# Optimization experiments

Measured on AMD Instinct MI355X. Metric: run time of the kernel, lower is better.

## Reference

```python
import jax, jax.numpy as jnp
import numpy as np

N = 50000      # nodes per graph
E = 800000     # edges per graph
IN_DIM = 64
HIDDEN = 128
OUT_DIM = 2
P = 100000     # candidate residue pairs


def setup_inputs() -> dict:
    key = jax.random.key(0)
    ks = jax.random.split(key, 12)
    x1 = jax.random.normal(ks[0], (N, IN_DIM), dtype=jnp.float32)
    x2 = jax.random.normal(ks[1], (N, IN_DIM), dtype=jnp.float32)
    edge_index1 = jax.random.randint(ks[2], (2, E), 0, N, dtype=jnp.int64)
    edge_index2 = jax.random.randint(ks[3], (2, E), 0, N, dtype=jnp.int64)
    label = jax.random.randint(ks[4], (P, 2), 0, N, dtype=jnp.int64)
    s = 0.05
    W0 = jax.random.normal(ks[5], (IN_DIM, HIDDEN), dtype=jnp.float32) * s
    W1 = jax.random.normal(ks[6], (HIDDEN, HIDDEN), dtype=jnp.float32) * s
    W2 = jax.random.normal(ks[7], (HIDDEN, HIDDEN), dtype=jnp.float32) * s
    b0 = jnp.zeros((HIDDEN,), dtype=jnp.float32)
    b1 = jnp.zeros((HIDDEN,), dtype=jnp.float32)
    b2 = jnp.zeros((HIDDEN,), dtype=jnp.float32)
    fcW = jax.random.normal(ks[8], (2 * HIDDEN, OUT_DIM), dtype=jnp.float32) * s
    fcb = jnp.zeros((OUT_DIM,), dtype=jnp.float32)
    return {"x1": x1, "edge_index1": edge_index1, "x2": x2,
            "edge_index2": edge_index2, "label": label,
            "W0": W0, "b0": b0, "W1": W1, "b1": b1, "W2": W2, "b2": b2,
            "fcW": fcW, "fcb": fcb}


def gcn_conv(x, src, dst, W, b):
    """PyG GCNConv: linear, add self-loops, symmetric D^-1/2 (A+I) D^-1/2 aggregation."""
    n = x.shape[0]
    h = x @ W                                   # [n, out]
    loops = jnp.arange(n, dtype=src.dtype)
    src_sl = jnp.concatenate([src, loops])      # [E+n]
    dst_sl = jnp.concatenate([dst, loops])
    deg = jax.ops.segment_sum(jnp.ones_like(src_sl, dtype=h.dtype), dst_sl,
                              num_segments=n)
    dinv = jax.lax.rsqrt(jnp.maximum(deg, 1.0e-12))
    norm = dinv[src_sl] * dinv[dst_sl]          # [E+n]
    msgs = h[src_sl] * norm[:, None]            # gather + scale
    out = jax.ops.segment_sum(msgs, dst_sl, num_segments=n)  # scatter-add
    return out + b


def gcn_tower(x, edge_index, params):
    src, dst = edge_index[0], edge_index[1]
    for (W, b) in params:
        x = jax.nn.relu(gcn_conv(x, src, dst, W, b))
    return x


def reference(x1, edge_index1, x2, edge_index2, label,
              W0, b0, W1, b1, W2, b2, fcW, fcb):
    params = [(W0, b0), (W1, b1), (W2, b2)]
    x_ligand = gcn_tower(x1, edge_index1, params)    # shared GCN weights
    x_receptor = gcn_tower(x2, edge_index2, params)
    x = jnp.concatenate([x_ligand[label[:, 0]], x_receptor[label[:, 1]]], axis=1)
    return jax.nn.relu(x @ fcW + fcb)
```

## Files before the change

kernel.cpp:

```cpp
#include <hip/hip_runtime.h>
#include <math.h>

typedef __attribute__((ext_vector_type(8))) short bf16x8;
typedef __attribute__((ext_vector_type(4))) float f32x4;

__device__ inline unsigned short f2bf(float f) {
    unsigned int u = __float_as_uint(f);
    unsigned int r = u + 0x7fffu + ((u >> 16) & 1u);
    return (unsigned short)(r >> 16);
}
__device__ inline float bf2f(unsigned short b) {
    return __uint_as_float(((unsigned int)b) << 16);
}


__global__ void histU_kernel(const int* __restrict__ d1, const int* __restrict__ d2,
                             int* __restrict__ cnt, int E, int N) {
    int i = blockIdx.x * blockDim.x + threadIdx.x;
    if (i < E) atomicAdd(&cnt[d1[i]], 1);
    else if (i < 2 * E) atomicAdd(&cnt[N + d2[i - E]], 1);
}

__global__ __launch_bounds__(256) void block_reduce_kernel(const int* __restrict__ cnt,
                                                           float* __restrict__ dinv,
                                                           int* __restrict__ blockSums, int NN) {
    int i = blockIdx.x * 256 + threadIdx.x;
    int v = 0;
    if (i < NN) {
        v = cnt[i];
        dinv[i] = 1.0f / sqrtf((float)(v + 1));
    }
    int s = v;
#pragma unroll
    for (int o = 32; o; o >>= 1) s += __shfl_down(s, o);
    __shared__ int ws[4];
    if ((threadIdx.x & 63) == 0) ws[threadIdx.x >> 6] = s;
    __syncthreads();
    if (threadIdx.x == 0) blockSums[blockIdx.x] = ws[0] + ws[1] + ws[2] + ws[3];
}

__global__ __launch_bounds__(1024) void scan_sums_kernel(const int* __restrict__ blockSums,
                                                         int* __restrict__ blockOff, int nb,
                                                         int* __restrict__ rowptr, int NN) {
    __shared__ int sh[1024];
    int t = threadIdx.x;
    int v = (t < nb) ? blockSums[t] : 0;
    sh[t] = v;
    __syncthreads();
    for (int o = 1; o < 1024; o <<= 1) {
        int u = (t >= o) ? sh[t - o] : 0;
        __syncthreads();
        sh[t] += u;
        __syncthreads();
    }
    if (t < nb) blockOff[t] = sh[t] - v;
    if (t == 1023) rowptr[NN] = sh[1023];
}

__global__ __launch_bounds__(256) void scan_write_kernel(const int* __restrict__ cnt,
                                                         const int* __restrict__ blockOff,
                                                         int* __restrict__ rowptr, int NN) {
    __shared__ int sh[256];
    int i = blockIdx.x * 256 + threadIdx.x;
    int t = threadIdx.x;
    int v = (i < NN) ? cnt[i] : 0;
    sh[t] = v;
    __syncthreads();
    for (int o = 1; o < 256; o <<= 1) {
        int u = (t >= o) ? sh[t - o] : 0;
        __syncthreads();
        sh[t] += u;
        __syncthreads();
    }
    if (i < NN) rowptr[i] = blockOff[blockIdx.x] + sh[t] - v;
}

__global__ void placeU_kernel(const int* __restrict__ s1, const int* __restrict__ d1,
                              const int* __restrict__ s2, const int* __restrict__ d2,
                              const int* __restrict__ rowptr, int* __restrict__ cnt,
                              int* __restrict__ csr, int E, int N) {
    int i = blockIdx.x * blockDim.x + threadIdx.x;
    int s, d;
    if (i < E)          { s = s1[i];         d = d1[i]; }
    else if (i < 2 * E) { s = s2[i - E] + N; d = d2[i - E] + N; }
    else return;
    int p = atomicSub(&cnt[d], 1);
    csr[rowptr[d] + p - 1] = s;
}


__global__ void prep_weights(const float* __restrict__ W0, const float* __restrict__ W1,
                             const float* __restrict__ W2,
                             unsigned short* __restrict__ W0h, unsigned short* __restrict__ W0l,
                             unsigned short* __restrict__ W1h, unsigned short* __restrict__ W1l,
                             unsigned short* __restrict__ W2h, unsigned short* __restrict__ W2l) {
    const float* W; unsigned short *Wh, *Wl; int K;
    if (blockIdx.x == 0)      { W = W0; Wh = W0h; Wl = W0l; K = 64; }
    else if (blockIdx.x == 1) { W = W1; Wh = W1h; Wl = W1l; K = 128; }
    else                      { W = W2; Wh = W2h; Wl = W2l; K = 128; }
    for (int i = threadIdx.x; i < K * 128; i += 256) {
        int k = i >> 7, c = i & 127;
        float v = W[i];
        unsigned short h = f2bf(v);
        unsigned short l = f2bf(v - bf2f(h));
        Wh[c * K + k] = h;
        Wl[c * K + k] = l;
    }
}


__global__ void prescale_kernel(const float* __restrict__ x1, const float* __restrict__ x2,
                                const float* __restrict__ dinv, float* __restrict__ X0, int NN,
                                int N) {
    int i = blockIdx.x * blockDim.x + threadIdx.x;
    if (i >= NN * 16) return;
    int r = i >> 4;
    const float4* src = (r < N) ? (const float4*)(x1) + i
                                : (const float4*)(x2) + (i - N * 16);
    float4 v = *src;
    float d = dinv[r];
    v.x *= d; v.y *= d; v.z *= d; v.w *= d;
    reinterpret_cast<float4*>(X0)[i] = v;
}


__global__ __launch_bounds__(512) void fused64_agg_gemm(
    const float* __restrict__ X, const int* __restrict__ rowptr,
    const int* __restrict__ csr,
    const unsigned short* __restrict__ WhT, const unsigned short* __restrict__ WlT,
    const float* __restrict__ bias, const float* __restrict__ dinv, int post,
    float* __restrict__ C, int M) {
    const int K = 64;
    const int LDA = K + 8;
    __shared__ unsigned short ldsH[64 * LDA];
    __shared__ unsigned short ldsL[64 * LDA];

    int t = threadIdx.x;
    int lane = t & 63, wid = t >> 6;
    int row0 = blockIdx.x * 64;

    const float4* X4 = (const float4*)X;
    int grp = lane >> 4;
    int fl = lane & 15;

    for (int rr = 0; rr < 2; ++rr) {
        int row = wid * 8 + rr * 4 + grp;
        int g = row0 + row; if (g >= M) g = M - 1;
        int beg = rowptr[g], end = rowptr[g + 1];
        float4 s4 = X4[(size_t)g * 16 + fl];
        float a0 = s4.x, a1 = s4.y, a2 = s4.z, a3 = s4.w;
        int e = beg;
        while (end - e >= 8) {
            int s0 = csr[e], s1 = csr[e + 1], s2 = csr[e + 2], s3 = csr[e + 3];
            int s4i = csr[e + 4], s5 = csr[e + 5], s6 = csr[e + 6], s7 = csr[e + 7];
            float4 v0 = X4[(size_t)s0 * 16 + fl];
            float4 v1 = X4[(size_t)s1 * 16 + fl];
            float4 v2 = X4[(size_t)s2 * 16 + fl];
            float4 v3 = X4[(size_t)s3 * 16 + fl];
            float4 v4 = X4[(size_t)s4i * 16 + fl];
            float4 v5 = X4[(size_t)s5 * 16 + fl];
            float4 v6 = X4[(size_t)s6 * 16 + fl];
            float4 v7 = X4[(size_t)s7 * 16 + fl];
            a0 += ((v0.x + v1.x) + (v2.x + v3.x)) + ((v4.x + v5.x) + (v6.x + v7.x));
            a1 += ((v0.y + v1.y) + (v2.y + v3.y)) + ((v4.y + v5.y) + (v6.y + v7.y));
            a2 += ((v0.z + v1.z) + (v2.z + v3.z)) + ((v4.z + v5.z) + (v6.z + v7.z));
            a3 += ((v0.w + v1.w) + (v2.w + v3.w)) + ((v4.w + v5.w) + (v6.w + v7.w));
            e += 8;
        }
        if (e < end) {
#pragma unroll
            for (int j = 0; j < 7; ++j) {
                int a = e + j;
                bool vld = a < end;
                int s = csr[vld ? a : beg];
                float m = vld ? 1.f : 0.f;
                float4 v = X4[(size_t)s * 16 + fl];
                a0 += m * v.x; a1 += m * v.y; a2 += m * v.z; a3 += m * v.w;
            }
        }
        ushort4 H, L;
        H.x = f2bf(a0); L.x = f2bf(a0 - bf2f(H.x));
        H.y = f2bf(a1); L.y = f2bf(a1 - bf2f(H.y));
        H.z = f2bf(a2); L.z = f2bf(a2 - bf2f(H.z));
        H.w = f2bf(a3); L.w = f2bf(a3 - bf2f(H.w));
        *reinterpret_cast<ushort4*>(&ldsH[row * LDA + fl * 4]) = H;
        *reinterpret_cast<ushort4*>(&ldsL[row * LDA + fl * 4]) = L;
    }
    __syncthreads();

    int c16 = lane & 15, kq = (lane >> 4) * 8;
    int col = wid * 16 + c16;

    bf16x8 wh[K / 32], wl[K / 32];
#pragma unroll
    for (int ks = 0; ks < K / 32; ++ks) {
        wh[ks] = *reinterpret_cast<const bf16x8*>(WhT + (size_t)col * K + ks * 32 + kq);
        wl[ks] = *reinterpret_cast<const bf16x8*>(WlT + (size_t)col * K + ks * 32 + kq);
    }
    float bb = bias[col];

#pragma unroll
    for (int rt = 0; rt < 4; ++rt) {
        f32x4 acc = {0.f, 0.f, 0.f, 0.f};
        int abase = (rt * 16 + c16) * LDA + kq;
#pragma unroll
        for (int ks = 0; ks < K / 32; ++ks) {
            bf16x8 ah = *reinterpret_cast<const bf16x8*>(ldsH + abase + ks * 32);
            bf16x8 al = *reinterpret_cast<const bf16x8*>(ldsL + abase + ks * 32);
            acc = __builtin_amdgcn_mfma_f32_16x16x32_bf16(ah, wh[ks], acc, 0, 0, 0);
            acc = __builtin_amdgcn_mfma_f32_16x16x32_bf16(ah, wl[ks], acc, 0, 0, 0);
            acc = __builtin_amdgcn_mfma_f32_16x16x32_bf16(al, wh[ks], acc, 0, 0, 0);
        }
#pragma unroll
        for (int r = 0; r < 4; ++r) {
            int gr = row0 + rt * 16 + (lane >> 4) * 4 + r;
            if (gr < M) {
                float d = dinv[gr];
                float po = post ? d : 1.0f;
                float v = fmaxf(acc[r] * d + bb, 0.f) * po;
                C[(size_t)gr * 128 + col] = v;
            }
        }
    }
}


__global__ __launch_bounds__(512) void fused128_agg_gemm(
    const float* __restrict__ X, const int* __restrict__ rowptr,
    const int* __restrict__ csr,
    const unsigned short* __restrict__ WhT, const unsigned short* __restrict__ WlT,
    const float* __restrict__ bias, const float* __restrict__ dinv, int post,
    float* __restrict__ C, int M) {
    const int K = 128;
    const int LDA = K + 8;
    __shared__ unsigned short ldsH[64 * LDA];
    __shared__ unsigned short ldsL[64 * LDA];

    int t = threadIdx.x;
    int lane = t & 63, wid = t >> 6;
    int row0 = blockIdx.x * 64;

    const float4* X4 = (const float4*)X;
    int grp = lane >> 5;
    int fl = lane & 31;

    for (int rr = 0; rr < 4; ++rr) {
        int row = wid * 8 + rr * 2 + grp;
        int g = row0 + row; if (g >= M) g = M - 1;
        int beg = rowptr[g], end = rowptr[g + 1];
        float4 s4 = X4[(size_t)g * 32 + fl];
        float a0 = s4.x, a1 = s4.y, a2 = s4.z, a3 = s4.w;
        int e = beg;
        while (end - e >= 8) {
            int s0 = csr[e], s1 = csr[e + 1], s2 = csr[e + 2], s3 = csr[e + 3];
            int s4i = csr[e + 4], s5 = csr[e + 5], s6 = csr[e + 6], s7 = csr[e + 7];
            float4 v0 = X4[(size_t)s0 * 32 + fl];
            float4 v1 = X4[(size_t)s1 * 32 + fl];
            float4 v2 = X4[(size_t)s2 * 32 + fl];
            float4 v3 = X4[(size_t)s3 * 32 + fl];
            float4 v4 = X4[(size_t)s4i * 32 + fl];
            float4 v5 = X4[(size_t)s5 * 32 + fl];
            float4 v6 = X4[(size_t)s6 * 32 + fl];
            float4 v7 = X4[(size_t)s7 * 32 + fl];
            a0 += ((v0.x + v1.x) + (v2.x + v3.x)) + ((v4.x + v5.x) + (v6.x + v7.x));
            a1 += ((v0.y + v1.y) + (v2.y + v3.y)) + ((v4.y + v5.y) + (v6.y + v7.y));
            a2 += ((v0.z + v1.z) + (v2.z + v3.z)) + ((v4.z + v5.z) + (v6.z + v7.z));
            a3 += ((v0.w + v1.w) + (v2.w + v3.w)) + ((v4.w + v5.w) + (v6.w + v7.w));
            e += 8;
        }
        if (e < end) {
#pragma unroll
            for (int j = 0; j < 7; ++j) {
                int a = e + j;
                bool vld = a < end;
                int s = csr[vld ? a : beg];
                float m = vld ? 1.f : 0.f;
                float4 v = X4[(size_t)s * 32 + fl];
                a0 += m * v.x; a1 += m * v.y; a2 += m * v.z; a3 += m * v.w;
            }
        }
        ushort4 H, L;
        H.x = f2bf(a0); L.x = f2bf(a0 - bf2f(H.x));
        H.y = f2bf(a1); L.y = f2bf(a1 - bf2f(H.y));
        H.z = f2bf(a2); L.z = f2bf(a2 - bf2f(H.z));
        H.w = f2bf(a3); L.w = f2bf(a3 - bf2f(H.w));
        *reinterpret_cast<ushort4*>(&ldsH[row * LDA + fl * 4]) = H;
        *reinterpret_cast<ushort4*>(&ldsL[row * LDA + fl * 4]) = L;
    }
    __syncthreads();

    int c16 = lane & 15, kq = (lane >> 4) * 8;
    int col = wid * 16 + c16;

    bf16x8 wh[K / 32], wl[K / 32];
#pragma unroll
    for (int ks = 0; ks < K / 32; ++ks) {
        wh[ks] = *reinterpret_cast<const bf16x8*>(WhT + (size_t)col * K + ks * 32 + kq);
        wl[ks] = *reinterpret_cast<const bf16x8*>(WlT + (size_t)col * K + ks * 32 + kq);
    }
    float bb = bias[col];

#pragma unroll
    for (int rt = 0; rt < 4; ++rt) {
        f32x4 acc = {0.f, 0.f, 0.f, 0.f};
        int abase = (rt * 16 + c16) * LDA + kq;
#pragma unroll
        for (int ks = 0; ks < K / 32; ++ks) {
            bf16x8 ah = *reinterpret_cast<const bf16x8*>(ldsH + abase + ks * 32);
            bf16x8 al = *reinterpret_cast<const bf16x8*>(ldsL + abase + ks * 32);
            acc = __builtin_amdgcn_mfma_f32_16x16x32_bf16(ah, wh[ks], acc, 0, 0, 0);
            acc = __builtin_amdgcn_mfma_f32_16x16x32_bf16(ah, wl[ks], acc, 0, 0, 0);
            acc = __builtin_amdgcn_mfma_f32_16x16x32_bf16(al, wh[ks], acc, 0, 0, 0);
        }
#pragma unroll
        for (int r = 0; r < 4; ++r) {
            int gr = row0 + rt * 16 + (lane >> 4) * 4 + r;
            if (gr < M) {
                float d = dinv[gr];
                float po = post ? d : 1.0f;
                float v = fmaxf(acc[r] * d + bb, 0.f) * po;
                C[(size_t)gr * 128 + col] = v;
            }
        }
    }
}


__global__ void fc_kernel(const float* __restrict__ H3, const int* __restrict__ label,
                          const float* __restrict__ fcW, const float* __restrict__ fcb,
                          float* __restrict__ out, int P, int N) {
    int w = blockIdx.x * (blockDim.x >> 6) + (threadIdx.x >> 6);
    int lane = threadIdx.x & 63;
    if (w >= P) return;
    int l0 = label[2 * w], l1 = label[2 * w + 1] + N;
    float xl0 = H3[(size_t)l0 * 128 + lane];
    float xl1 = H3[(size_t)l0 * 128 + 64 + lane];
    float xr0 = H3[(size_t)l1 * 128 + lane];
    float xr1 = H3[(size_t)l1 * 128 + 64 + lane];
    float a0 = xl0 * fcW[lane * 2]             + xl1 * fcW[(64 + lane) * 2]
             + xr0 * fcW[(128 + lane) * 2]     + xr1 * fcW[(192 + lane) * 2];
    float a1 = xl0 * fcW[lane * 2 + 1]         + xl1 * fcW[(64 + lane) * 2 + 1]
             + xr0 * fcW[(128 + lane) * 2 + 1] + xr1 * fcW[(192 + lane) * 2 + 1];
#pragma unroll
    for (int o = 32; o; o >>= 1) {
        a0 += __shfl_xor(a0, o);
        a1 += __shfl_xor(a1, o);
    }
    if (lane == 0) {
        out[2 * w]     = fmaxf(a0 + fcb[0], 0.f);
        out[2 * w + 1] = fmaxf(a1 + fcb[1], 0.f);
    }
}


extern "C" void kernel_launch(void* const* d_in, const int* in_sizes, int n_in,
                              void* d_out, int out_size, void* d_ws, size_t ws_size,
                              hipStream_t stream) {
    const float* x1   = (const float*)d_in[0];
    const int*   e1   = (const int*)d_in[1];
    const float* x2   = (const float*)d_in[2];
    const int*   e2   = (const int*)d_in[3];
    const int*   label= (const int*)d_in[4];
    const float* W0   = (const float*)d_in[5];
    const float* b0   = (const float*)d_in[6];
    const float* W1   = (const float*)d_in[7];
    const float* b1   = (const float*)d_in[8];
    const float* W2   = (const float*)d_in[9];
    const float* b2   = (const float*)d_in[10];
    const float* fcW  = (const float*)d_in[11];
    const float* fcb  = (const float*)d_in[12];
    float* out = (float*)d_out;

    const int N = in_sizes[0] / 64;
    const int E = in_sizes[1] / 2;
    const int P = in_sizes[4] / 2;
    const int NN = 2 * N;
    const int NB = (NN + 255) / 256;
    const int GB = (NN + 63) / 64;

    char* ws = (char*)d_ws;
    size_t off = 0;
    auto alloc = [&](size_t bytes) -> void* {
        void* p = ws + off;
        off += (bytes + 255) & ~(size_t)255;
        return p;
    };
    int*   cnt      = (int*)alloc((size_t)NN * 4);
    int*   rowptr   = (int*)alloc((size_t)(NN + 1) * 4);
    float* dinv     = (float*)alloc((size_t)NN * 4);
    int*   csr      = (int*)alloc((size_t)2 * E * 4);
    int*   blockSums= (int*)alloc((size_t)NB * 4);
    int*   blockOff = (int*)alloc((size_t)NB * 4);
    float* bufA     = (float*)alloc((size_t)NN * 128 * 4);
    float* bufB     = (float*)alloc((size_t)NN * 128 * 4);
    unsigned short* W0h = (unsigned short*)alloc(64 * 128 * 2);
    unsigned short* W0l = (unsigned short*)alloc(64 * 128 * 2);
    unsigned short* W1h = (unsigned short*)alloc(128 * 128 * 2);
    unsigned short* W1l = (unsigned short*)alloc(128 * 128 * 2);
    unsigned short* W2h = (unsigned short*)alloc(128 * 128 * 2);
    unsigned short* W2l = (unsigned short*)alloc(128 * 128 * 2);

    prep_weights<<<3, 256, 0, stream>>>(W0, W1, W2, W0h, W0l, W1h, W1l, W2h, W2l);

    hipMemsetAsync(cnt, 0, (size_t)NN * 4, stream);
    histU_kernel<<<(2 * E + 255) / 256, 256, 0, stream>>>(e1 + E, e2 + E, cnt, E, N);
    block_reduce_kernel<<<NB, 256, 0, stream>>>(cnt, dinv, blockSums, NN);
    scan_sums_kernel<<<1, 1024, 0, stream>>>(blockSums, blockOff, NB, rowptr, NN);
    scan_write_kernel<<<NB, 256, 0, stream>>>(cnt, blockOff, rowptr, NN);
    placeU_kernel<<<(2 * E + 255) / 256, 256, 0, stream>>>(e1, e1 + E, e2, e2 + E,
                                                           rowptr, cnt, csr, E, N);
    prescale_kernel<<<(NN * 16 + 255) / 256, 256, 0, stream>>>(x1, x2, dinv, bufA, NN, N);
    fused64_agg_gemm<<<GB, 512, 0, stream>>>(bufA, rowptr, csr, W0h, W0l, b0, dinv, 1,
                                             bufB, NN);
    fused128_agg_gemm<<<GB, 512, 0, stream>>>(bufB, rowptr, csr, W1h, W1l, b1, dinv, 1,
                                              bufA, NN);
    fused128_agg_gemm<<<GB, 512, 0, stream>>>(bufA, rowptr, csr, W2h, W2l, b2, dinv, 0,
                                              bufB, NN);

    fc_kernel<<<(P + 3) / 4, 256, 0, stream>>>(bufB, label, fcW, fcb, out, P, N);
}
```

Before: 539.7 us.

## Make fused aggregation-GEMM kernels persistent with an atomic tile counter

Both fused aggregate+GEMM kernels become persistent. A capped grid of blocks repeatedly claims 64-row tiles through a global atomic counter, which is zeroed by extending the existing histogram memset. The aim is to even out load imbalance from varying node degrees and to cut block launch and tail overhead. In exchange it adds one atomic and one extra block-wide barrier per tile, and still reloads the weight fragments for every tile.

```diff
diff --git a/kernel.cpp b/kernel.cpp
--- a/kernel.cpp
+++ b/kernel.cpp
@@ -129,96 +129,104 @@
     const int* __restrict__ csr,
     const unsigned short* __restrict__ WhT, const unsigned short* __restrict__ WlT,
     const float* __restrict__ bias, const float* __restrict__ dinv, int post,
-    float* __restrict__ C, int M) {
+    float* __restrict__ C, int M, int* __restrict__ tileCtr, int nTiles) {
     const int K = 64;
     const int LDA = K + 8;
     __shared__ unsigned short ldsH[64 * LDA];
     __shared__ unsigned short ldsL[64 * LDA];
+    __shared__ int sTile;
 
     int t = threadIdx.x;
     int lane = t & 63, wid = t >> 6;
-    int row0 = blockIdx.x * 64;
 
     const float4* X4 = (const float4*)X;
     int grp = lane >> 4;
     int fl = lane & 15;
 
-    for (int rr = 0; rr < 2; ++rr) {
-        int row = wid * 8 + rr * 4 + grp;
-        int g = row0 + row; if (g >= M) g = M - 1;
-        int beg = rowptr[g], end = rowptr[g + 1];
-        float4 s4 = X4[(size_t)g * 16 + fl];
-        float a0 = s4.x, a1 = s4.y, a2 = s4.z, a3 = s4.w;
-        int e = beg;
-        while (end - e >= 8) {
-            int s0 = csr[e], s1 = csr[e + 1], s2 = csr[e + 2], s3 = csr[e + 3];
-            int s4i = csr[e + 4], s5 = csr[e + 5], s6 = csr[e + 6], s7 = csr[e + 7];
-            float4 v0 = X4[(size_t)s0 * 16 + fl];
-            float4 v1 = X4[(size_t)s1 * 16 + fl];
-            float4 v2 = X4[(size_t)s2 * 16 + fl];
-            float4 v3 = X4[(size_t)s3 * 16 + fl];
-            float4 v4 = X4[(size_t)s4i * 16 + fl];
-            float4 v5 = X4[(size_t)s5 * 16 + fl];
-            float4 v6 = X4[(size_t)s6 * 16 + fl];
-            float4 v7 = X4[(size_t)s7 * 16 + fl];
-            a0 += ((v0.x + v1.x) + (v2.x + v3.x)) + ((v4.x + v5.x) + (v6.x + v7.x));
-            a1 += ((v0.y + v1.y) + (v2.y + v3.y)) + ((v4.y + v5.y) + (v6.y + v7.y));
-            a2 += ((v0.z + v1.z) + (v2.z + v3.z)) + ((v4.z + v5.z) + (v6.z + v7.z));
-            a3 += ((v0.w + v1.w) + (v2.w + v3.w)) + ((v4.w + v5.w) + (v6.w + v7.w));
-            e += 8;
-        }
-        if (e < end) {
-#pragma unroll
-            for (int j = 0; j < 7; ++j) {
-                int a = e + j;
-                bool vld = a < end;
-                int s = csr[vld ? a : beg];
-                float m = vld ? 1.f : 0.f;
-                float4 v = X4[(size_t)s * 16 + fl];
-                a0 += m * v.x; a1 += m * v.y; a2 += m * v.z; a3 += m * v.w;
-            }
-        }
-        ushort4 H, L;
-        H.x = f2bf(a0); L.x = f2bf(a0 - bf2f(H.x));
-        H.y = f2bf(a1); L.y = f2bf(a1 - bf2f(H.y));
-        H.z = f2bf(a2); L.z = f2bf(a2 - bf2f(H.z));
-        H.w = f2bf(a3); L.w = f2bf(a3 - bf2f(H.w));
-        *reinterpret_cast<ushort4*>(&ldsH[row * LDA + fl * 4]) = H;
-        *reinterpret_cast<ushort4*>(&ldsL[row * LDA + fl * 4]) = L;
-    }
-    __syncthreads();
-
     int c16 = lane & 15, kq = (lane >> 4) * 8;
     int col = wid * 16 + c16;
 
-    bf16x8 wh[K / 32], wl[K / 32];
-#pragma unroll
-    for (int ks = 0; ks < K / 32; ++ks) {
-        wh[ks] = *reinterpret_cast<const bf16x8*>(WhT + (size_t)col * K + ks * 32 + kq);
-        wl[ks] = *reinterpret_cast<const bf16x8*>(WlT + (size_t)col * K + ks * 32 + kq);
-    }
-    float bb = bias[col];
-
-#pragma unroll
-    for (int rt = 0; rt < 4; ++rt) {
-        f32x4 acc = {0.f, 0.f, 0.f, 0.f};
-        int abase = (rt * 16 + c16) * LDA + kq;
+    while (true) {
+        if (t == 0) sTile = atomicAdd(tileCtr, 1);
+        __syncthreads();
+        int tile = sTile;
+        if (tile >= nTiles) return;
+        int row0 = tile * 64;
+
+        for (int rr = 0; rr < 2; ++rr) {
+            int row = wid * 8 + rr * 4 + grp;
+            int g = row0 + row; if (g >= M) g = M - 1;
+            int beg = rowptr[g], end = rowptr[g + 1];
+            float4 s4 = X4[(size_t)g * 16 + fl];
+            float a0 = s4.x, a1 = s4.y, a2 = s4.z, a3 = s4.w;
+            int e = beg;
+            while (end - e >= 8) {
+                int s0 = csr[e], s1 = csr[e + 1], s2 = csr[e + 2], s3 = csr[e + 3];
+                int s4i = csr[e + 4], s5 = csr[e + 5], s6 = csr[e + 6], s7 = csr[e + 7];
+                float4 v0 = X4[(size_t)s0 * 16 + fl];
+                float4 v1 = X4[(size_t)s1 * 16 + fl];
+                float4 v2 = X4[(size_t)s2 * 16 + fl];
+                float4 v3 = X4[(size_t)s3 * 16 + fl];
+                float4 v4 = X4[(size_t)s4i * 16 + fl];
+                float4 v5 = X4[(size_t)s5 * 16 + fl];
+                float4 v6 = X4[(size_t)s6 * 16 + fl];
+                float4 v7 = X4[(size_t)s7 * 16 + fl];
+                a0 += ((v0.x + v1.x) + (v2.x + v3.x)) + ((v4.x + v5.x) + (v6.x + v7.x));
+                a1 += ((v0.y + v1.y) + (v2.y + v3.y)) + ((v4.y + v5.y) + (v6.y + v7.y));
+                a2 += ((v0.z + v1.z) + (v2.z + v3.z)) + ((v4.z + v5.z) + (v6.z + v7.z));
+                a3 += ((v0.w + v1.w) + (v2.w + v3.w)) + ((v4.w + v5.w) + (v6.w + v7.w));
+                e += 8;
+            }
+            if (e < end) {
+#pragma unroll
+                for (int j = 0; j < 7; ++j) {
+                    int a = e + j;
+                    bool vld = a < end;
+                    int s = csr[vld ? a : beg];
+                    float m = vld ? 1.f : 0.f;
+                    float4 v = X4[(size_t)s * 16 + fl];
+                    a0 += m * v.x; a1 += m * v.y; a2 += m * v.z; a3 += m * v.w;
+                }
+            }
+            ushort4 H, L;
+            H.x = f2bf(a0); L.x = f2bf(a0 - bf2f(H.x));
+            H.y = f2bf(a1); L.y = f2bf(a1 - bf2f(H.y));
+            H.z = f2bf(a2); L.z = f2bf(a2 - bf2f(H.z));
+            H.w = f2bf(a3); L.w = f2bf(a3 - bf2f(H.w));
+            *reinterpret_cast<ushort4*>(&ldsH[row * LDA + fl * 4]) = H;
+            *reinterpret_cast<ushort4*>(&ldsL[row * LDA + fl * 4]) = L;
+        }
+        __syncthreads();
+
+        bf16x8 wh[K / 32], wl[K / 32];
 #pragma unroll
         for (int ks = 0; ks < K / 32; ++ks) {
-            bf16x8 ah = *reinterpret_cast<const bf16x8*>(ldsH + abase + ks * 32);
-            bf16x8 al = *reinterpret_cast<const bf16x8*>(ldsL + abase + ks * 32);
-            acc = __builtin_amdgcn_mfma_f32_16x16x32_bf16(ah, wh[ks], acc, 0, 0, 0);
-            acc = __builtin_amdgcn_mfma_f32_16x16x32_bf16(ah, wl[ks], acc, 0, 0, 0);
-            acc = __builtin_amdgcn_mfma_f32_16x16x32_bf16(al, wh[ks], acc, 0, 0, 0);
-        }
-#pragma unroll
-        for (int r = 0; r < 4; ++r) {
-            int gr = row0 + rt * 16 + (lane >> 4) * 4 + r;
-            if (gr < M) {
-                float d = dinv[gr];
-                float po = post ? d : 1.0f;
-                float v = fmaxf(acc[r] * d + bb, 0.f) * po;
-                C[(size_t)gr * 128 + col] = v;
+            wh[ks] = *reinterpret_cast<const bf16x8*>(WhT + (size_t)col * K + ks * 32 + kq);
+            wl[ks] = *reinterpret_cast<const bf16x8*>(WlT + (size_t)col * K + ks * 32 + kq);
+        }
+        float bb = bias[col];
+
+#pragma unroll
+        for (int rt = 0; rt < 4; ++rt) {
+            f32x4 acc = {0.f, 0.f, 0.f, 0.f};
+            int abase = (rt * 16 + c16) * LDA + kq;
+#pragma unroll
+            for (int ks = 0; ks < K / 32; ++ks) {
+                bf16x8 ah = *reinterpret_cast<const bf16x8*>(ldsH + abase + ks * 32);
+                bf16x8 al = *reinterpret_cast<const bf16x8*>(ldsL + abase + ks * 32);
+                acc = __builtin_amdgcn_mfma_f32_16x16x32_bf16(ah, wh[ks], acc, 0, 0, 0);
+                acc = __builtin_amdgcn_mfma_f32_16x16x32_bf16(ah, wl[ks], acc, 0, 0, 0);
+                acc = __builtin_amdgcn_mfma_f32_16x16x32_bf16(al, wh[ks], acc, 0, 0, 0);
+            }
+#pragma unroll
+            for (int r = 0; r < 4; ++r) {
+                int gr = row0 + rt * 16 + (lane >> 4) * 4 + r;
+                if (gr < M) {
+                    float d = dinv[gr];
+                    float po = post ? d : 1.0f;
+                    float v = fmaxf(acc[r] * d + bb, 0.f) * po;
+                    C[(size_t)gr * 128 + col] = v;
+                }
             }
         }
     }
@@ -230,96 +238,104 @@
     const int* __restrict__ csr,
     const unsigned short* __restrict__ WhT, const unsigned short* __restrict__ WlT,
     const float* __restrict__ bias, const float* __restrict__ dinv, int post,
-    float* __restrict__ C, int M) {
+    float* __restrict__ C, int M, int* __restrict__ tileCtr, int nTiles) {
     const int K = 128;
     const int LDA = K + 8;
     __shared__ unsigned short ldsH[64 * LDA];
     __shared__ unsigned short ldsL[64 * LDA];
+    __shared__ int sTile;
 
     int t = threadIdx.x;
     int lane = t & 63, wid = t >> 6;
-    int row0 = blockIdx.x * 64;
 
     const float4* X4 = (const float4*)X;
     int grp = lane >> 5;
     int fl = lane & 31;
 
-    for (int rr = 0; rr < 4; ++rr) {
-        int row = wid * 8 + rr * 2 + grp;
-        int g = row0 + row; if (g >= M) g = M - 1;
-        int beg = rowptr[g], end = rowptr[g + 1];
-        float4 s4 = X4[(size_t)g * 32 + fl];
-        float a0 = s4.x, a1 = s4.y, a2 = s4.z, a3 = s4.w;
-        int e = beg;
-        while (end - e >= 8) {
-            int s0 = csr[e], s1 = csr[e + 1], s2 = csr[e + 2], s3 = csr[e + 3];
-            int s4i = csr[e + 4], s5 = csr[e + 5], s6 = csr[e + 6], s7 = csr[e + 7];
-            float4 v0 = X4[(size_t)s0 * 32 + fl];
-            float4 v1 = X4[(size_t)s1 * 32 + fl];
-            float4 v2 = X4[(size_t)s2 * 32 + fl];
-            float4 v3 = X4[(size_t)s3 * 32 + fl];
-            float4 v4 = X4[(size_t)s4i * 32 + fl];
-            float4 v5 = X4[(size_t)s5 * 32 + fl];
-            float4 v6 = X4[(size_t)s6 * 32 + fl];
-            float4 v7 = X4[(size_t)s7 * 32 + fl];
-            a0 += ((v0.x + v1.x) + (v2.x + v3.x)) + ((v4.x + v5.x) + (v6.x + v7.x));
-            a1 += ((v0.y + v1.y) + (v2.y + v3.y)) + ((v4.y + v5.y) + (v6.y + v7.y));
-            a2 += ((v0.z + v1.z) + (v2.z + v3.z)) + ((v4.z + v5.z) + (v6.z + v7.z));
-            a3 += ((v0.w + v1.w) + (v2.w + v3.w)) + ((v4.w + v5.w) + (v6.w + v7.w));
-            e += 8;
-        }
-        if (e < end) {
-#pragma unroll
-            for (int j = 0; j < 7; ++j) {
-                int a = e + j;
-                bool vld = a < end;
-                int s = csr[vld ? a : beg];
-                float m = vld ? 1.f : 0.f;
-                float4 v = X4[(size_t)s * 32 + fl];
-                a0 += m * v.x; a1 += m * v.y; a2 += m * v.z; a3 += m * v.w;
-            }
-        }
-        ushort4 H, L;
-        H.x = f2bf(a0); L.x = f2bf(a0 - bf2f(H.x));
-        H.y = f2bf(a1); L.y = f2bf(a1 - bf2f(H.y));
-        H.z = f2bf(a2); L.z = f2bf(a2 - bf2f(H.z));
-        H.w = f2bf(a3); L.w = f2bf(a3 - bf2f(H.w));
-        *reinterpret_cast<ushort4*>(&ldsH[row * LDA + fl * 4]) = H;
-        *reinterpret_cast<ushort4*>(&ldsL[row * LDA + fl * 4]) = L;
-    }
-    __syncthreads();
-
     int c16 = lane & 15, kq = (lane >> 4) * 8;
     int col = wid * 16 + c16;
 
-    bf16x8 wh[K / 32], wl[K / 32];
-#pragma unroll
-    for (int ks = 0; ks < K / 32; ++ks) {
-        wh[ks] = *reinterpret_cast<const bf16x8*>(WhT + (size_t)col * K + ks * 32 + kq);
-        wl[ks] = *reinterpret_cast<const bf16x8*>(WlT + (size_t)col * K + ks * 32 + kq);
-    }
-    float bb = bias[col];
-
-#pragma unroll
-    for (int rt = 0; rt < 4; ++rt) {
-        f32x4 acc = {0.f, 0.f, 0.f, 0.f};
-        int abase = (rt * 16 + c16) * LDA + kq;
+    while (true) {
+        if (t == 0) sTile = atomicAdd(tileCtr, 1);
+        __syncthreads();
+        int tile = sTile;
+        if (tile >= nTiles) return;
+        int row0 = tile * 64;
+
+        for (int rr = 0; rr < 4; ++rr) {
+            int row = wid * 8 + rr * 2 + grp;
+            int g = row0 + row; if (g >= M) g = M - 1;
+            int beg = rowptr[g], end = rowptr[g + 1];
+            float4 s4 = X4[(size_t)g * 32 + fl];
+            float a0 = s4.x, a1 = s4.y, a2 = s4.z, a3 = s4.w;
+            int e = beg;
+            while (end - e >= 8) {
+                int s0 = csr[e], s1 = csr[e + 1], s2 = csr[e + 2], s3 = csr[e + 3];
+                int s4i = csr[e + 4], s5 = csr[e + 5], s6 = csr[e + 6], s7 = csr[e + 7];
+                float4 v0 = X4[(size_t)s0 * 32 + fl];
+                float4 v1 = X4[(size_t)s1 * 32 + fl];
+                float4 v2 = X4[(size_t)s2 * 32 + fl];
+                float4 v3 = X4[(size_t)s3 * 32 + fl];
+                float4 v4 = X4[(size_t)s4i * 32 + fl];
+                float4 v5 = X4[(size_t)s5 * 32 + fl];
+                float4 v6 = X4[(size_t)s6 * 32 + fl];
+                float4 v7 = X4[(size_t)s7 * 32 + fl];
+                a0 += ((v0.x + v1.x) + (v2.x + v3.x)) + ((v4.x + v5.x) + (v6.x + v7.x));
+                a1 += ((v0.y + v1.y) + (v2.y + v3.y)) + ((v4.y + v5.y) + (v6.y + v7.y));
+                a2 += ((v0.z + v1.z) + (v2.z + v3.z)) + ((v4.z + v5.z) + (v6.z + v7.z));
+                a3 += ((v0.w + v1.w) + (v2.w + v3.w)) + ((v4.w + v5.w) + (v6.w + v7.w));
+                e += 8;
+            }
+            if (e < end) {
+#pragma unroll
+                for (int j = 0; j < 7; ++j) {
+                    int a = e + j;
+                    bool vld = a < end;
+                    int s = csr[vld ? a : beg];
+                    float m = vld ? 1.f : 0.f;
+                    float4 v = X4[(size_t)s * 32 + fl];
+                    a0 += m * v.x; a1 += m * v.y; a2 += m * v.z; a3 += m * v.w;
+                }
+            }
+            ushort4 H, L;
+            H.x = f2bf(a0); L.x = f2bf(a0 - bf2f(H.x));
+            H.y = f2bf(a1); L.y = f2bf(a1 - bf2f(H.y));
+            H.z = f2bf(a2); L.z = f2bf(a2 - bf2f(H.z));
+            H.w = f2bf(a3); L.w = f2bf(a3 - bf2f(H.w));
+            *reinterpret_cast<ushort4*>(&ldsH[row * LDA + fl * 4]) = H;
+            *reinterpret_cast<ushort4*>(&ldsL[row * LDA + fl * 4]) = L;
+        }
+        __syncthreads();
+
+        bf16x8 wh[K / 32], wl[K / 32];
 #pragma unroll
         for (int ks = 0; ks < K / 32; ++ks) {
-            bf16x8 ah = *reinterpret_cast<const bf16x8*>(ldsH + abase + ks * 32);
-            bf16x8 al = *reinterpret_cast<const bf16x8*>(ldsL + abase + ks * 32);
-            acc = __builtin_amdgcn_mfma_f32_16x16x32_bf16(ah, wh[ks], acc, 0, 0, 0);
-            acc = __builtin_amdgcn_mfma_f32_16x16x32_bf16(ah, wl[ks], acc, 0, 0, 0);
-            acc = __builtin_amdgcn_mfma_f32_16x16x32_bf16(al, wh[ks], acc, 0, 0, 0);
-        }
-#pragma unroll
-        for (int r = 0; r < 4; ++r) {
-            int gr = row0 + rt * 16 + (lane >> 4) * 4 + r;
-            if (gr < M) {
-                float d = dinv[gr];
-                float po = post ? d : 1.0f;
-                float v = fmaxf(acc[r] * d + bb, 0.f) * po;
-                C[(size_t)gr * 128 + col] = v;
+            wh[ks] = *reinterpret_cast<const bf16x8*>(WhT + (size_t)col * K + ks * 32 + kq);
+            wl[ks] = *reinterpret_cast<const bf16x8*>(WlT + (size_t)col * K + ks * 32 + kq);
+        }
+        float bb = bias[col];
+
+#pragma unroll
+        for (int rt = 0; rt < 4; ++rt) {
+            f32x4 acc = {0.f, 0.f, 0.f, 0.f};
+            int abase = (rt * 16 + c16) * LDA + kq;
+#pragma unroll
+            for (int ks = 0; ks < K / 32; ++ks) {
+                bf16x8 ah = *reinterpret_cast<const bf16x8*>(ldsH + abase + ks * 32);
+                bf16x8 al = *reinterpret_cast<const bf16x8*>(ldsL + abase + ks * 32);
+                acc = __builtin_amdgcn_mfma_f32_16x16x32_bf16(ah, wh[ks], acc, 0, 0, 0);
+                acc = __builtin_amdgcn_mfma_f32_16x16x32_bf16(ah, wl[ks], acc, 0, 0, 0);
+                acc = __builtin_amdgcn_mfma_f32_16x16x32_bf16(al, wh[ks], acc, 0, 0, 0);
+            }
+#pragma unroll
+            for (int r = 0; r < 4; ++r) {
+                int gr = row0 + rt * 16 + (lane >> 4) * 4 + r;
+                if (gr < M) {
+                    float d = dinv[gr];
+                    float po = post ? d : 1.0f;
+                    float v = fmaxf(acc[r] * d + bb, 0.f) * po;
+                    C[(size_t)gr * 128 + col] = v;
+                }
             }
         }
     }
@@ -377,6 +393,8 @@
     const int NN = 2 * N;
     const int NB = (NN + 255) / 256;
     const int GB = (NN + 63) / 64;
+    const int PB64 = (GB < 2048) ? GB : 2048;
+    const int PB128 = (GB < 1024) ? GB : 1024;
 
     char* ws = (char*)d_ws;
     size_t off = 0;
@@ -385,7 +403,7 @@
         off += (bytes + 255) & ~(size_t)255;
         return p;
     };
-    int*   cnt      = (int*)alloc((size_t)NN * 4);
+    int*   cnt      = (int*)alloc((size_t)(NN + 16) * 4);
     int*   rowptr   = (int*)alloc((size_t)(NN + 1) * 4);
     float* dinv     = (float*)alloc((size_t)NN * 4);
     int*   csr      = (int*)alloc((size_t)2 * E * 4);
@@ -399,10 +417,11 @@
     unsigned short* W1l = (unsigned short*)alloc(128 * 128 * 2);
     unsigned short* W2h = (unsigned short*)alloc(128 * 128 * 2);
     unsigned short* W2l = (unsigned short*)alloc(128 * 128 * 2);
+    int* ctr = cnt + NN;
 
     prep_weights<<<3, 256, 0, stream>>>(W0, W1, W2, W0h, W0l, W1h, W1l, W2h, W2l);
 
-    hipMemsetAsync(cnt, 0, (size_t)NN * 4, stream);
+    hipMemsetAsync(cnt, 0, (size_t)(NN + 16) * 4, stream);
     histU_kernel<<<(2 * E + 255) / 256, 256, 0, stream>>>(e1 + E, e2 + E, cnt, E, N);
     block_reduce_kernel<<<NB, 256, 0, stream>>>(cnt, dinv, blockSums, NN);
     scan_sums_kernel<<<1, 1024, 0, stream>>>(blockSums, blockOff, NB, rowptr, NN);
@@ -410,12 +429,12 @@
     placeU_kernel<<<(2 * E + 255) / 256, 256, 0, stream>>>(e1, e1 + E, e2, e2 + E,
                                                            rowptr, cnt, csr, E, N);
     prescale_kernel<<<(NN * 16 + 255) / 256, 256, 0, stream>>>(x1, x2, dinv, bufA, NN, N);
-    fused64_agg_gemm<<<GB, 512, 0, stream>>>(bufA, rowptr, csr, W0h, W0l, b0, dinv, 1,
-                                             bufB, NN);
-    fused128_agg_gemm<<<GB, 512, 0, stream>>>(bufB, rowptr, csr, W1h, W1l, b1, dinv, 1,
-                                              bufA, NN);
-    fused128_agg_gemm<<<GB, 512, 0, stream>>>(bufA, rowptr, csr, W2h, W2l, b2, dinv, 0,
-                                              bufB, NN);
+    fused64_agg_gemm<<<PB64, 512, 0, stream>>>(bufA, rowptr, csr, W0h, W0l, b0, dinv, 1,
+                                               bufB, NN, ctr + 0, GB);
+    fused128_agg_gemm<<<PB128, 512, 0, stream>>>(bufB, rowptr, csr, W1h, W1l, b1, dinv, 1,
+                                                 bufA, NN, ctr + 1, GB);
+    fused128_agg_gemm<<<PB128, 512, 0, stream>>>(bufA, rowptr, csr, W2h, W2l, b2, dinv, 0,
+                                                 bufB, NN, ctr + 2, GB);
 
     fc_kernel<<<(P + 3) / 4, 256, 0, stream>>>(bufB, label, fcW, fcb, out, P, N);
 }
```

Result: slower. 577.0 us (+6.9%).
